# Performance work log

Hardware: AMD Instinct MI355X
Metric: run time of the kernel (lower is better)

Reference implementation:

```python
import jax, jax.numpy as jnp
import numpy as np

N_NODES = 100000
N_EDGES = 1600000
IN_CH, HID_CH, OUT_CH = 128, 128, 64


def glorot(key, fan_in, fan_out):
    lim = np.sqrt(6.0 / (fan_in + fan_out)).astype(np.float32)
    return jax.random.uniform(key, (fan_in, fan_out), jnp.float32, -lim, lim)


def gcn_conv(x, src, dst, W, b):
    """PyG GCNConv: add self-loops, symmetric deg^-1/2 normalization,
    linear transform, scatter-add aggregation at targets, plus bias."""
    n = x.shape[0]
    xw = x @ W  # [N, F_out]
    loop = jnp.arange(n)
    s = jnp.concatenate([src, loop])  # sources (message origin)
    d = jnp.concatenate([dst, loop])  # targets (aggregation site)
    deg = jax.ops.segment_sum(jnp.ones_like(d, dtype=xw.dtype), d, num_segments=n)
    dinv = jnp.where(deg > 0, jax.lax.rsqrt(deg), 0.0)
    norm = dinv[s] * dinv[d]  # [E+N]
    out = jax.ops.segment_sum(norm[:, None] * xw[s], d, num_segments=n)
    return out + b


def setup_inputs() -> dict:
    key = jax.random.key(0)
    ks = jax.random.split(key, 8)
    x = jax.random.normal(ks[0], (N_NODES, IN_CH), jnp.float32)
    edge_index = jax.random.randint(ks[1], (2, N_EDGES), 0, N_NODES, jnp.int64)
    return {
        "x": x,
        "edge_index": edge_index,
        "W1": glorot(ks[2], IN_CH, HID_CH),
        "b1": jnp.zeros((HID_CH,), jnp.float32),
        "W2": glorot(ks[3], HID_CH, HID_CH),
        "b2": jnp.zeros((HID_CH,), jnp.float32),
        "W3": glorot(ks[4], HID_CH, OUT_CH),
        "b3": jnp.zeros((OUT_CH,), jnp.float32),
    }


def reference(x, edge_index, W1, b1, W2, b2, W3, b3):
    src, dst = edge_index[0], edge_index[1]
    # eval mode: dropout is identity
    h = jax.nn.relu(gcn_conv(x, src, dst, W1, b1))
    h = jax.nn.relu(gcn_conv(h, src, dst, W2, b2))
    h = gcn_conv(h, src, dst, W3, b3)
    return jax.nn.log_softmax(h, axis=1)
```

## Files before the change

kernel.cpp:

```cpp
#include <hip/hip_runtime.h>
#include <math.h>


#define NN 100000
#define NE 1600000
#define NBUK 391
#define BCAP 4608

typedef float floatx4 __attribute__((ext_vector_type(4)));
typedef short short8 __attribute__((ext_vector_type(8)));

__device__ __forceinline__ unsigned short f2bf(float f) {
    unsigned u = __float_as_uint(f);
    unsigned r = (u + 0x7fffu + ((u >> 16) & 1u)) >> 16;
    return (unsigned short)r;
}
__device__ __forceinline__ float bflo(unsigned u) { return __uint_as_float(u << 16); }
__device__ __forceinline__ float bfhi(unsigned u) { return __uint_as_float(u & 0xffff0000u); }

__global__ __launch_bounds__(256) void k_f2bf(const float4* __restrict__ in, uint4* __restrict__ out, int ngroups) {
    int i = blockIdx.x * 256 + threadIdx.x;
    if (i >= ngroups) return;
    float4 a = in[i * 2], b = in[i * 2 + 1];
    uint4 o;
    o.x = ((unsigned)f2bf(a.y) << 16) | f2bf(a.x);
    o.y = ((unsigned)f2bf(a.w) << 16) | f2bf(a.z);
    o.z = ((unsigned)f2bf(b.y) << 16) | f2bf(b.x);
    o.w = ((unsigned)f2bf(b.w) << 16) | f2bf(b.z);
    out[i] = o;
}


__global__ __launch_bounds__(256) void k_bucket(const int* __restrict__ src, const int* __restrict__ dst,
                                                int* __restrict__ bcur, int* __restrict__ bbuf, int E) {
    __shared__ int hist[NBUK];
    __shared__ int base[NBUK];
    int t = threadIdx.x;
    for (int b = t; b < NBUK; b += 256) hist[b] = 0;
    __syncthreads();
    int e0 = blockIdx.x * 4096;
    #pragma unroll
    for (int j = 0; j < 16; j++) {
        int e = e0 + j * 256 + t;
        if (e < E) atomicAdd(&hist[dst[e] >> 8], 1);
    }
    __syncthreads();
    for (int b = t; b < NBUK; b += 256) {
        int c = hist[b];
        base[b] = c ? atomicAdd(&bcur[b], c) : 0;
        hist[b] = 0;
    }
    __syncthreads();
    #pragma unroll
    for (int j = 0; j < 16; j++) {
        int e = e0 + j * 256 + t;
        if (e < E) {
            int d = dst[e];
            int b = d >> 8;
            int r = atomicAdd(&hist[b], 1);
            int pos = base[b] + r;
            if (pos < BCAP) bbuf[b * BCAP + pos] = (src[e] << 8) | (d & 255);
        }
    }
}

__global__ void k_scanbuckets(const int* __restrict__ bcur, int* __restrict__ bbase, int nb,
                              int* __restrict__ row_ptr, int n, int E) {
    int lane = threadIdx.x;
    int carry = 0;
    for (int base = 0; base < nb; base += 64) {
        int idx = base + lane;
        int v = (idx < nb) ? min(bcur[idx], BCAP) : 0;
        int orig = v;
        #pragma unroll
        for (int o = 1; o < 64; o <<= 1) {
            int u = __shfl_up(v, o);
            if (lane >= o) v += u;
        }
        if (idx < nb) bbase[idx] = carry + v - orig;
        carry += __shfl(v, 63);
    }
    if (lane == 0) row_ptr[n] = E;
}


__global__ __launch_bounds__(256) void k_build(const int* __restrict__ bcur, const int* __restrict__ bbase,
                                               const int* __restrict__ bbuf,
                                               int* __restrict__ row_ptr, int* __restrict__ csr, int N) {
    __shared__ int sh[256];
    __shared__ int cur[256];
    __shared__ int loc[BCAP];
    int b = blockIdx.x, t = threadIdx.x;
    int cnt = min(bcur[b], BCAP);
    int gbase = bbase[b];
    const int* bp = bbuf + b * BCAP;
    sh[t] = 0;
    __syncthreads();
    for (int i = t; i < cnt; i += 256) atomicAdd(&sh[bp[i] & 255], 1);
    __syncthreads();
    int v = sh[t];
    for (int o = 1; o < 256; o <<= 1) {
        int u = (t >= o) ? sh[t - o] : 0;
        __syncthreads();
        sh[t] += u;
        __syncthreads();
    }
    int excl = sh[t] - v;
    int node = b * 256 + t;
    if (node < N) row_ptr[node] = gbase + excl;
    cur[t] = excl;
    __syncthreads();
    for (int i = t; i < cnt; i += 256) {
        int p = bp[i];
        int r = atomicAdd(&cur[p & 255], 1);
        loc[r] = p >> 8;
    }
    __syncthreads();
    for (int i = t; i < cnt; i += 256) csr[gbase + i] = loc[i];
}

__global__ __launch_bounds__(256) void k_dinv(const int* __restrict__ row_ptr, float* __restrict__ dinv, int n) {
    int i = blockIdx.x * 256 + threadIdx.x;
    if (i < n) {
        int d = row_ptr[i + 1] - row_ptr[i];
        dinv[i] = rsqrtf((float)d + 1.0f);
    }
}


template <int NC>
__global__ __launch_bounds__(256) void k_mfma(const unsigned short* __restrict__ A, const float* __restrict__ W,
                                              const float* __restrict__ dinv, unsigned short* __restrict__ Y, int M) {
    constexpr int K = 128;
    constexpr int NT = NC / 16;
    __shared__ unsigned short Wt[NC][136];
    int t = threadIdx.x;
    for (int idx = t; idx < K * NC; idx += 256) {
        int k = idx / NC, n = idx % NC;
        Wt[n][k] = f2bf(W[idx]);
    }
    __syncthreads();
    int lane = t & 63;
    int wid = t >> 6;
    int col = lane & 15;
    int quad = lane >> 4;
    int nstrips = M / 16;
    for (int s = blockIdx.x * 4 + wid; s < nstrips; s += gridDim.x * 4) {
        int row0 = s * 16;
        floatx4 acc[NT];
        #pragma unroll
        for (int i = 0; i < NT; i++) acc[i] = (floatx4){0.f, 0.f, 0.f, 0.f};
        #pragma unroll
        for (int ks = 0; ks < 4; ks++) {
            const unsigned short* ap = A + (size_t)(row0 + col) * K + ks * 32 + quad * 8;
            short8 afrag = *(const short8*)ap;
            #pragma unroll
            for (int nt = 0; nt < NT; nt++) {
                short8 bfrag = *(const short8*)&Wt[nt * 16 + col][ks * 32 + quad * 8];
                acc[nt] = __builtin_amdgcn_mfma_f32_16x16x32_bf16(afrag, bfrag, acc[nt], 0, 0, 0);
            }
        }
        #pragma unroll
        for (int r = 0; r < 4; r++) {
            int row = row0 + quad * 4 + r;
            float dv = dinv[row];
            #pragma unroll
            for (int nt = 0; nt < NT; nt++) {
                Y[(size_t)row * NC + nt * 16 + col] = f2bf(acc[nt][r] * dv);
            }
        }
    }
}


__device__ __forceinline__ void acc8(float* a, uint4 v) {
    a[0] += bflo(v.x); a[1] += bfhi(v.x);
    a[2] += bflo(v.y); a[3] += bfhi(v.y);
    a[4] += bflo(v.z); a[5] += bfhi(v.z);
    a[6] += bflo(v.w); a[7] += bfhi(v.w);
}

__global__ __launch_bounds__(256) void k_gather_relu_bf(const uint4* __restrict__ y, const int* __restrict__ csr,
                                                        const int* __restrict__ row_ptr, const float* __restrict__ dinv,
                                                        const float* __restrict__ bias, uint4* __restrict__ h, int n) {
    int node = blockIdx.x * 16 + (threadIdx.x >> 4);
    int c = threadIdx.x & 15;
    if (node >= n) return;
    int s0 = row_ptr[node], s1 = row_ptr[node + 1];
    float a[8] = {};
    acc8(a, y[(size_t)node * 16 + c]);
    int p = s0;
    for (; p + 4 <= s1; p += 4) {
        int i0 = csr[p], i1 = csr[p + 1], i2 = csr[p + 2], i3 = csr[p + 3];
        uint4 v0 = y[(size_t)i0 * 16 + c];
        uint4 v1 = y[(size_t)i1 * 16 + c];
        uint4 v2 = y[(size_t)i2 * 16 + c];
        uint4 v3 = y[(size_t)i3 * 16 + c];
        acc8(a, v0); acc8(a, v1); acc8(a, v2); acc8(a, v3);
    }
    for (; p < s1; p++) acc8(a, y[(size_t)csr[p] * 16 + c]);
    float s = dinv[node];
    float4 b0 = ((const float4*)bias)[c * 2];
    float4 b1 = ((const float4*)bias)[c * 2 + 1];
    float r0 = fmaxf(s * a[0] + b0.x, 0.f), r1 = fmaxf(s * a[1] + b0.y, 0.f);
    float r2 = fmaxf(s * a[2] + b0.z, 0.f), r3 = fmaxf(s * a[3] + b0.w, 0.f);
    float r4 = fmaxf(s * a[4] + b1.x, 0.f), r5 = fmaxf(s * a[5] + b1.y, 0.f);
    float r6 = fmaxf(s * a[6] + b1.z, 0.f), r7 = fmaxf(s * a[7] + b1.w, 0.f);
    uint4 o;
    o.x = ((unsigned)f2bf(r1) << 16) | f2bf(r0);
    o.y = ((unsigned)f2bf(r3) << 16) | f2bf(r2);
    o.z = ((unsigned)f2bf(r5) << 16) | f2bf(r4);
    o.w = ((unsigned)f2bf(r7) << 16) | f2bf(r6);
    h[(size_t)node * 16 + c] = o;
}

__global__ __launch_bounds__(256) void k_gather_lsm_bf(const uint4* __restrict__ y, const int* __restrict__ csr,
                                                       const int* __restrict__ row_ptr, const float* __restrict__ dinv,
                                                       const float* __restrict__ bias, float4* __restrict__ out4, int n) {
    int node = blockIdx.x * 32 + (threadIdx.x >> 3);
    int c = threadIdx.x & 7;
    if (node >= n) return;
    int s0 = row_ptr[node], s1 = row_ptr[node + 1];
    float a[8] = {};
    acc8(a, y[(size_t)node * 8 + c]);
    int p = s0;
    for (; p + 4 <= s1; p += 4) {
        int i0 = csr[p], i1 = csr[p + 1], i2 = csr[p + 2], i3 = csr[p + 3];
        uint4 v0 = y[(size_t)i0 * 8 + c];
        uint4 v1 = y[(size_t)i1 * 8 + c];
        uint4 v2 = y[(size_t)i2 * 8 + c];
        uint4 v3 = y[(size_t)i3 * 8 + c];
        acc8(a, v0); acc8(a, v1); acc8(a, v2); acc8(a, v3);
    }
    for (; p < s1; p++) acc8(a, y[(size_t)csr[p] * 8 + c]);
    float s = dinv[node];
    float4 b0 = ((const float4*)bias)[c * 2];
    float4 b1 = ((const float4*)bias)[c * 2 + 1];
    float v[8];
    v[0] = s * a[0] + b0.x; v[1] = s * a[1] + b0.y; v[2] = s * a[2] + b0.z; v[3] = s * a[3] + b0.w;
    v[4] = s * a[4] + b1.x; v[5] = s * a[5] + b1.y; v[6] = s * a[6] + b1.z; v[7] = s * a[7] + b1.w;
    float m = v[0];
    #pragma unroll
    for (int i = 1; i < 8; i++) m = fmaxf(m, v[i]);
    #pragma unroll
    for (int o = 4; o > 0; o >>= 1) m = fmaxf(m, __shfl_xor(m, o));
    float sum = 0.f;
    #pragma unroll
    for (int i = 0; i < 8; i++) sum += expf(v[i] - m);
    #pragma unroll
    for (int o = 4; o > 0; o >>= 1) sum += __shfl_xor(sum, o);
    float lse = m + logf(sum);
    out4[(size_t)node * 16 + c * 2]     = make_float4(v[0] - lse, v[1] - lse, v[2] - lse, v[3] - lse);
    out4[(size_t)node * 16 + c * 2 + 1] = make_float4(v[4] - lse, v[5] - lse, v[6] - lse, v[7] - lse);
}


extern "C" void kernel_launch(void* const* d_in, const int* in_sizes, int n_in,
                              void* d_out, int out_size, void* d_ws, size_t ws_size,
                              hipStream_t stream) {
    const float* x  = (const float*)d_in[0];
    const int*   ei = (const int*)d_in[1];
    const float* W1 = (const float*)d_in[2];
    const float* b1 = (const float*)d_in[3];
    const float* W2 = (const float*)d_in[4];
    const float* b2 = (const float*)d_in[5];
    const float* W3 = (const float*)d_in[6];
    const float* b3 = (const float*)d_in[7];
    float* out = (float*)d_out;

    const int N = NN, E = NE;
    const int nb = (N + 255) / 256;

    char* ws = (char*)d_ws;
    size_t off = 0;
    auto alloc = [&](size_t bytes) -> void* {
        void* p = ws + off;
        off += bytes;
        off = (off + 255) & ~(size_t)255;
        return p;
    };
    int*            row_ptr = (int*)alloc((size_t)(N + 1) * 4);
    float*          dinvv   = (float*)alloc((size_t)N * 4);
    int*            bcur    = (int*)alloc(512 * 4);
    int*            bbase   = (int*)alloc(512 * 4);
    int*            bbuf    = (int*)alloc((size_t)NBUK * BCAP * 4);
    int*            csr     = (int*)alloc((size_t)E * 4);
    unsigned short* xb      = (unsigned short*)alloc((size_t)N * 128 * 2);
    unsigned short* yb      = (unsigned short*)alloc((size_t)N * 128 * 2);
    unsigned short* hb      = (unsigned short*)alloc((size_t)N * 128 * 2);
    (void)ws_size; (void)in_sizes; (void)n_in; (void)out_size;

    const int* srcp = ei;
    const int* dstp = ei + E;

    hipMemsetAsync(bcur, 0, 512 * 4, stream);
    k_f2bf<<<(N * 128 / 8 + 255) / 256, 256, 0, stream>>>((const float4*)x, (uint4*)xb, N * 128 / 8);
    k_bucket<<<(E + 4095) / 4096, 256, 0, stream>>>(srcp, dstp, bcur, bbuf, E);
    k_scanbuckets<<<1, 64, 0, stream>>>(bcur, bbase, NBUK, row_ptr, N, E);
    k_build<<<NBUK, 256, 0, stream>>>(bcur, bbase, bbuf, row_ptr, csr, N);
    k_dinv<<<nb, 256, 0, stream>>>(row_ptr, dinvv, N);

    k_mfma<128><<<512, 256, 0, stream>>>(xb, W1, dinvv, yb, N);
    k_gather_relu_bf<<<N / 16, 256, 0, stream>>>((const uint4*)yb, csr, row_ptr, dinvv, b1, (uint4*)hb, N);
    k_mfma<128><<<512, 256, 0, stream>>>(hb, W2, dinvv, yb, N);
    k_gather_relu_bf<<<N / 16, 256, 0, stream>>>((const uint4*)yb, csr, row_ptr, dinvv, b2, (uint4*)hb, N);
    k_mfma<64><<<512, 256, 0, stream>>>(hb, W3, dinvv, yb, N);
    k_gather_lsm_bf<<<N / 32, 256, 0, stream>>>((const uint4*)yb, csr, row_ptr, dinvv, b3, (float4*)out, N);
}
```

Before: 358.6 us.

## Fuse input bf16 cast into first GEMM, pre-transpose weights, vectorize bucketing, prefetch gather indices

```diff
diff --git a/kernel.cpp b/kernel.cpp
--- a/kernel.cpp
+++ b/kernel.cpp
@@ -18,31 +18,33 @@
 __device__ __forceinline__ float bflo(unsigned u) { return __uint_as_float(u << 16); }
 __device__ __forceinline__ float bfhi(unsigned u) { return __uint_as_float(u & 0xffff0000u); }
 
-__global__ __launch_bounds__(256) void k_f2bf(const float4* __restrict__ in, uint4* __restrict__ out, int ngroups) {
-    int i = blockIdx.x * 256 + threadIdx.x;
-    if (i >= ngroups) return;
-    float4 a = in[i * 2], b = in[i * 2 + 1];
-    uint4 o;
-    o.x = ((unsigned)f2bf(a.y) << 16) | f2bf(a.x);
-    o.y = ((unsigned)f2bf(a.w) << 16) | f2bf(a.z);
-    o.z = ((unsigned)f2bf(b.y) << 16) | f2bf(b.x);
-    o.w = ((unsigned)f2bf(b.w) << 16) | f2bf(b.z);
-    out[i] = o;
-}
-
-
-__global__ __launch_bounds__(256) void k_bucket(const int* __restrict__ src, const int* __restrict__ dst,
+__global__ __launch_bounds__(256) void k_wprep(const float* __restrict__ W, unsigned short* __restrict__ Wtg,
+                                               int K, int NC) {
+    int idx = blockIdx.x * 256 + threadIdx.x;
+    if (idx >= NC * K) return;
+    int n = idx / K, k = idx - n * K;
+    Wtg[idx] = f2bf(W[k * NC + n]);
+}
+
+__global__ __launch_bounds__(256) void k_bucket(const int4* __restrict__ src4, const int4* __restrict__ dst4,
                                                 int* __restrict__ bcur, int* __restrict__ bbuf, int E) {
     __shared__ int hist[NBUK];
     __shared__ int base[NBUK];
     int t = threadIdx.x;
     for (int b = t; b < NBUK; b += 256) hist[b] = 0;
     __syncthreads();
-    int e0 = blockIdx.x * 4096;
-    #pragma unroll
-    for (int j = 0; j < 16; j++) {
-        int e = e0 + j * 256 + t;
-        if (e < E) atomicAdd(&hist[dst[e] >> 8], 1);
+    int E4 = E >> 2;
+    int q0 = blockIdx.x * 1024;
+    #pragma unroll
+    for (int j = 0; j < 4; j++) {
+        int q = q0 + j * 256 + t;
+        if (q < E4) {
+            int4 d = dst4[q];
+            atomicAdd(&hist[d.x >> 8], 1);
+            atomicAdd(&hist[d.y >> 8], 1);
+            atomicAdd(&hist[d.z >> 8], 1);
+            atomicAdd(&hist[d.w >> 8], 1);
+        }
     }
     __syncthreads();
     for (int b = t; b < NBUK; b += 256) {
@@ -52,14 +54,20 @@
     }
     __syncthreads();
     #pragma unroll
-    for (int j = 0; j < 16; j++) {
-        int e = e0 + j * 256 + t;
-        if (e < E) {
-            int d = dst[e];
-            int b = d >> 8;
-            int r = atomicAdd(&hist[b], 1);
-            int pos = base[b] + r;
-            if (pos < BCAP) bbuf[b * BCAP + pos] = (src[e] << 8) | (d & 255);
+    for (int j = 0; j < 4; j++) {
+        int q = q0 + j * 256 + t;
+        if (q < E4) {
+            int4 s = src4[q];
+            int4 d = dst4[q];
+            int sv[4] = {s.x, s.y, s.z, s.w};
+            int dv[4] = {d.x, d.y, d.z, d.w};
+            #pragma unroll
+            for (int u = 0; u < 4; u++) {
+                int b = dv[u] >> 8;
+                int r = atomicAdd(&hist[b], 1);
+                int pos = base[b] + r;
+                if (pos < BCAP) bbuf[b * BCAP + pos] = (sv[u] << 8) | (dv[u] & 255);
+            }
         }
     }
 }
@@ -82,7 +90,6 @@
     }
     if (lane == 0) row_ptr[n] = E;
 }
-
 
 __global__ __launch_bounds__(256) void k_build(const int* __restrict__ bcur, const int* __restrict__ bbase,
                                                const int* __restrict__ bbuf,
@@ -128,46 +135,63 @@
 }
 
 
-template <int NC>
-__global__ __launch_bounds__(256) void k_mfma(const unsigned short* __restrict__ A, const float* __restrict__ W,
+template <int NC, bool CVT>
+__global__ __launch_bounds__(256) void k_mfma(const void* __restrict__ Av, const unsigned short* __restrict__ Wtg,
                                               const float* __restrict__ dinv, unsigned short* __restrict__ Y, int M) {
     constexpr int K = 128;
     constexpr int NT = NC / 16;
     __shared__ unsigned short Wt[NC][136];
     int t = threadIdx.x;
-    for (int idx = t; idx < K * NC; idx += 256) {
-        int k = idx / NC, n = idx % NC;
-        Wt[n][k] = f2bf(W[idx]);
-    }
-    __syncthreads();
-    int lane = t & 63;
-    int wid = t >> 6;
-    int col = lane & 15;
-    int quad = lane >> 4;
+    constexpr int NV = NC * K / 8;
+    for (int idx = t; idx < NV; idx += 256) {
+        int nrow = idx >> 4;
+        int chunk = idx & 15;
+        *(uint4*)&Wt[nrow][chunk * 8] = *(const uint4*)(Wtg + nrow * K + chunk * 8);
+    }
+    __syncthreads();
+    int lane = t & 63, wid = t >> 6;
+    int col = lane & 15, quad = lane >> 4;
     int nstrips = M / 16;
-    for (int s = blockIdx.x * 4 + wid; s < nstrips; s += gridDim.x * 4) {
-        int row0 = s * 16;
-        floatx4 acc[NT];
-        #pragma unroll
-        for (int i = 0; i < NT; i++) acc[i] = (floatx4){0.f, 0.f, 0.f, 0.f};
+    int s = blockIdx.x * 4 + wid;
+    if (s >= nstrips) return;
+    int row0 = s * 16;
+
+    short8 af[4];
+    if (CVT) {
+        const float* Af = (const float*)Av + (size_t)(row0 + col) * K + quad * 8;
         #pragma unroll
         for (int ks = 0; ks < 4; ks++) {
-            const unsigned short* ap = A + (size_t)(row0 + col) * K + ks * 32 + quad * 8;
-            short8 afrag = *(const short8*)ap;
-            #pragma unroll
-            for (int nt = 0; nt < NT; nt++) {
-                short8 bfrag = *(const short8*)&Wt[nt * 16 + col][ks * 32 + quad * 8];
-                acc[nt] = __builtin_amdgcn_mfma_f32_16x16x32_bf16(afrag, bfrag, acc[nt], 0, 0, 0);
-            }
-        }
-        #pragma unroll
-        for (int r = 0; r < 4; r++) {
-            int row = row0 + quad * 4 + r;
-            float dv = dinv[row];
-            #pragma unroll
-            for (int nt = 0; nt < NT; nt++) {
-                Y[(size_t)row * NC + nt * 16 + col] = f2bf(acc[nt][r] * dv);
-            }
+            float4 f0 = *(const float4*)(Af + ks * 32);
+            float4 f1 = *(const float4*)(Af + ks * 32 + 4);
+            short8 v;
+            v[0] = (short)f2bf(f0.x); v[1] = (short)f2bf(f0.y); v[2] = (short)f2bf(f0.z); v[3] = (short)f2bf(f0.w);
+            v[4] = (short)f2bf(f1.x); v[5] = (short)f2bf(f1.y); v[6] = (short)f2bf(f1.z); v[7] = (short)f2bf(f1.w);
+            af[ks] = v;
+        }
+    } else {
+        const unsigned short* Ab = (const unsigned short*)Av + (size_t)(row0 + col) * K + quad * 8;
+        #pragma unroll
+        for (int ks = 0; ks < 4; ks++) af[ks] = *(const short8*)(Ab + ks * 32);
+    }
+
+    floatx4 acc[NT];
+    #pragma unroll
+    for (int i = 0; i < NT; i++) acc[i] = (floatx4){0.f, 0.f, 0.f, 0.f};
+    #pragma unroll
+    for (int ks = 0; ks < 4; ks++) {
+        #pragma unroll
+        for (int nt = 0; nt < NT; nt++) {
+            short8 bfrag = *(const short8*)&Wt[nt * 16 + col][ks * 32 + quad * 8];
+            acc[nt] = __builtin_amdgcn_mfma_f32_16x16x32_bf16(af[ks], bfrag, acc[nt], 0, 0, 0);
+        }
+    }
+    #pragma unroll
+    for (int r = 0; r < 4; r++) {
+        int row = row0 + quad * 4 + r;
+        float dv = dinv[row];
+        #pragma unroll
+        for (int nt = 0; nt < NT; nt++) {
+            Y[(size_t)row * NC + nt * 16 + col] = f2bf(acc[nt][r] * dv);
         }
     }
 }
@@ -190,13 +214,32 @@
     float a[8] = {};
     acc8(a, y[(size_t)node * 16 + c]);
     int p = s0;
-    for (; p + 4 <= s1; p += 4) {
-        int i0 = csr[p], i1 = csr[p + 1], i2 = csr[p + 2], i3 = csr[p + 3];
-        uint4 v0 = y[(size_t)i0 * 16 + c];
-        uint4 v1 = y[(size_t)i1 * 16 + c];
-        uint4 v2 = y[(size_t)i2 * 16 + c];
-        uint4 v3 = y[(size_t)i3 * 16 + c];
+    int i0, i1, i2, i3, i4, i5, i6, i7;
+    if (p + 8 <= s1) {
+        i0 = csr[p]; i1 = csr[p+1]; i2 = csr[p+2]; i3 = csr[p+3];
+        i4 = csr[p+4]; i5 = csr[p+5]; i6 = csr[p+6]; i7 = csr[p+7];
+        while (true) {
+            uint4 v0 = y[(size_t)i0 * 16 + c], v1 = y[(size_t)i1 * 16 + c];
+            uint4 v2 = y[(size_t)i2 * 16 + c], v3 = y[(size_t)i3 * 16 + c];
+            uint4 v4 = y[(size_t)i4 * 16 + c], v5 = y[(size_t)i5 * 16 + c];
+            uint4 v6 = y[(size_t)i6 * 16 + c], v7 = y[(size_t)i7 * 16 + c];
+            p += 8;
+            bool nxt = (p + 8 <= s1);
+            if (nxt) {
+                i0 = csr[p]; i1 = csr[p+1]; i2 = csr[p+2]; i3 = csr[p+3];
+                i4 = csr[p+4]; i5 = csr[p+5]; i6 = csr[p+6]; i7 = csr[p+7];
+            }
+            acc8(a, v0); acc8(a, v1); acc8(a, v2); acc8(a, v3);
+            acc8(a, v4); acc8(a, v5); acc8(a, v6); acc8(a, v7);
+            if (!nxt) break;
+        }
+    }
+    if (p + 4 <= s1) {
+        int j0 = csr[p], j1 = csr[p+1], j2 = csr[p+2], j3 = csr[p+3];
+        uint4 v0 = y[(size_t)j0 * 16 + c], v1 = y[(size_t)j1 * 16 + c];
+        uint4 v2 = y[(size_t)j2 * 16 + c], v3 = y[(size_t)j3 * 16 + c];
         acc8(a, v0); acc8(a, v1); acc8(a, v2); acc8(a, v3);
+        p += 4;
     }
     for (; p < s1; p++) acc8(a, y[(size_t)csr[p] * 16 + c]);
     float s = dinv[node];
@@ -224,13 +267,32 @@
     float a[8] = {};
     acc8(a, y[(size_t)node * 8 + c]);
     int p = s0;
-    for (; p + 4 <= s1; p += 4) {
-        int i0 = csr[p], i1 = csr[p + 1], i2 = csr[p + 2], i3 = csr[p + 3];
-        uint4 v0 = y[(size_t)i0 * 8 + c];
-        uint4 v1 = y[(size_t)i1 * 8 + c];
-        uint4 v2 = y[(size_t)i2 * 8 + c];
-        uint4 v3 = y[(size_t)i3 * 8 + c];
+    int i0, i1, i2, i3, i4, i5, i6, i7;
+    if (p + 8 <= s1) {
+        i0 = csr[p]; i1 = csr[p+1]; i2 = csr[p+2]; i3 = csr[p+3];
+        i4 = csr[p+4]; i5 = csr[p+5]; i6 = csr[p+6]; i7 = csr[p+7];
+        while (true) {
+            uint4 v0 = y[(size_t)i0 * 8 + c], v1 = y[(size_t)i1 * 8 + c];
+            uint4 v2 = y[(size_t)i2 * 8 + c], v3 = y[(size_t)i3 * 8 + c];
+            uint4 v4 = y[(size_t)i4 * 8 + c], v5 = y[(size_t)i5 * 8 + c];
+            uint4 v6 = y[(size_t)i6 * 8 + c], v7 = y[(size_t)i7 * 8 + c];
+            p += 8;
+            bool nxt = (p + 8 <= s1);
+            if (nxt) {
+                i0 = csr[p]; i1 = csr[p+1]; i2 = csr[p+2]; i3 = csr[p+3];
+                i4 = csr[p+4]; i5 = csr[p+5]; i6 = csr[p+6]; i7 = csr[p+7];
+            }
+            acc8(a, v0); acc8(a, v1); acc8(a, v2); acc8(a, v3);
+            acc8(a, v4); acc8(a, v5); acc8(a, v6); acc8(a, v7);
+            if (!nxt) break;
+        }
+    }
+    if (p + 4 <= s1) {
+        int j0 = csr[p], j1 = csr[p+1], j2 = csr[p+2], j3 = csr[p+3];
+        uint4 v0 = y[(size_t)j0 * 8 + c], v1 = y[(size_t)j1 * 8 + c];
+        uint4 v2 = y[(size_t)j2 * 8 + c], v3 = y[(size_t)j3 * 8 + c];
         acc8(a, v0); acc8(a, v1); acc8(a, v2); acc8(a, v3);
+        p += 4;
     }
     for (; p < s1; p++) acc8(a, y[(size_t)csr[p] * 8 + c]);
     float s = dinv[node];
@@ -285,7 +347,9 @@
     int*            bbase   = (int*)alloc(512 * 4);
     int*            bbuf    = (int*)alloc((size_t)NBUK * BCAP * 4);
     int*            csr     = (int*)alloc((size_t)E * 4);
-    unsigned short* xb      = (unsigned short*)alloc((size_t)N * 128 * 2);
+    unsigned short* wt1     = (unsigned short*)alloc(128 * 128 * 2);
+    unsigned short* wt2     = (unsigned short*)alloc(128 * 128 * 2);
+    unsigned short* wt3     = (unsigned short*)alloc(64 * 128 * 2);
     unsigned short* yb      = (unsigned short*)alloc((size_t)N * 128 * 2);
     unsigned short* hb      = (unsigned short*)alloc((size_t)N * 128 * 2);
     (void)ws_size; (void)in_sizes; (void)n_in; (void)out_size;
@@ -294,16 +358,20 @@
     const int* dstp = ei + E;
 
     hipMemsetAsync(bcur, 0, 512 * 4, stream);
-    k_f2bf<<<(N * 128 / 8 + 255) / 256, 256, 0, stream>>>((const float4*)x, (uint4*)xb, N * 128 / 8);
-    k_bucket<<<(E + 4095) / 4096, 256, 0, stream>>>(srcp, dstp, bcur, bbuf, E);
+    k_wprep<<<64, 256, 0, stream>>>(W1, wt1, 128, 128);
+    k_wprep<<<64, 256, 0, stream>>>(W2, wt2, 128, 128);
+    k_wprep<<<32, 256, 0, stream>>>(W3, wt3, 128, 64);
+    k_bucket<<<(E + 4095) / 4096, 256, 0, stream>>>((const int4*)srcp, (const int4*)dstp, bcur, bbuf, E);
     k_scanbuckets<<<1, 64, 0, stream>>>(bcur, bbase, NBUK, row_ptr, N, E);
     k_build<<<NBUK, 256, 0, stream>>>(bcur, bbase, bbuf, row_ptr, csr, N);
     k_dinv<<<nb, 256, 0, stream>>>(row_ptr, dinvv, N);
 
-    k_mfma<128><<<512, 256, 0, stream>>>(xb, W1, dinvv, yb, N);
+    const int nstrips = N / 16;
+    const int gmm = (nstrips + 3) / 4;
+    k_mfma<128, true><<<gmm, 256, 0, stream>>>(x, wt1, dinvv, yb, N);
     k_gather_relu_bf<<<N / 16, 256, 0, stream>>>((const uint4*)yb, csr, row_ptr, dinvv, b1, (uint4*)hb, N);
-    k_mfma<128><<<512, 256, 0, stream>>>(hb, W2, dinvv, yb, N);
+    k_mfma<128, false><<<gmm, 256, 0, stream>>>(hb, wt2, dinvv, yb, N);
     k_gather_relu_bf<<<N / 16, 256, 0, stream>>>((const uint4*)yb, csr, row_ptr, dinvv, b2, (uint4*)hb, N);
-    k_mfma<64><<<512, 256, 0, stream>>>(hb, W3, dinvv, yb, N);
+    k_mfma<64, false><<<gmm, 256, 0, stream>>>(hb, wt3, dinvv, yb, N);
     k_gather_lsm_bf<<<N / 32, 256, 0, stream>>>((const uint4*)yb, csr, row_ptr, dinvv, b3, (float4*)out, N);
 }
```

Measured after the change: 342.3 us. 1.05x faster.
